# Optimization experiments

Hardware: AMD Instinct MI355X
Metric: run time of the kernel (lower is better)

Reference implementation:

```python
import jax, jax.numpy as jnp
import numpy as np
from math import factorial

# ---- static config: mirrors FullTensorProductSparse("64x0e + 64x1o", "32x0e + 32x1o", leading_shape=(2048,)) ----
IRREPS1 = [(64, 0, 1), (64, 1, -1)]   # (mul, l, parity); already regrouped
IRREPS2 = [(32, 0, 1), (32, 1, -1)]
N_LEAD = 2048


def _su2_cg_coeff(j1, m1, j2, m2, j3, m3):
    # Racah formula, identical to e3nn._su2_clebsch_gordan_coeff
    if m3 != m1 + m2:
        return 0.0
    f = factorial
    vmin = max(-j1 + j2 + m3, -j1 + m1, 0)
    vmax = min(j2 + j3 + m1, j3 - j1 + j2, j3 + m3)
    C = ((2.0 * j3 + 1.0) * f(j3 + j1 - j2) * f(j3 - j1 + j2) * f(j1 + j2 - j3)
         * f(j3 + m3) * f(j3 - m3)
         / (f(j1 + j2 + j3 + 1) * f(j1 - m1) * f(j1 + m1) * f(j2 - m2) * f(j2 + m2))) ** 0.5
    S = 0.0
    for v in range(vmin, vmax + 1):
        S += (-1.0) ** (v + j2 + m2) * f(j2 + j3 + m1 - v) * f(j1 - m1 + v) / (
            f(v) * f(j3 - j1 + j2 - v) * f(j3 + m3 - v) * f(v + j1 - j2 - m3))
    return C * S


def _su2_cg(j1, j2, j3):
    mat = np.zeros((2 * j1 + 1, 2 * j2 + 1, 2 * j3 + 1), dtype=np.float64)
    if abs(j1 - j2) <= j3 <= j1 + j2:
        for m1 in range(-j1, j1 + 1):
            for m2 in range(-j2, j2 + 1):
                if abs(m1 + m2) <= j3:
                    mat[j1 + m1, j2 + m2, j3 + m1 + m2] = _su2_cg_coeff(j1, m1, j2, m2, j3, m1 + m2)
    return mat / (2 * j3 + 1) ** 0.5


def _change_basis_real_to_complex(l):
    q = np.zeros((2 * l + 1, 2 * l + 1), dtype=np.complex128)
    for m in range(-l, 0):
        q[l + m, l + abs(m)] = 2 ** -0.5
        q[l + m, l - abs(m)] = -1j * 2 ** -0.5
    q[l, l] = 1.0
    for m in range(1, l + 1):
        q[l + m, l + abs(m)] = (-1) ** m * 2 ** -0.5
        q[l + m, l - abs(m)] = 1j * (-1) ** m * 2 ** -0.5
    return (-1j) ** l * q  # phase makes the real-basis CG coefficients real


def wigner_3j(l1, l2, l3):
    # real-basis Wigner 3j, identical to e3nn.o3.wigner_3j
    Q1 = _change_basis_real_to_complex(l1)
    Q2 = _change_basis_real_to_complex(l2)
    Q3 = _change_basis_real_to_complex(l3)
    C = _su2_cg(l1, l2, l3).astype(np.complex128)
    C = np.einsum('ij,kl,mn,ikn->jlm', Q1, Q2, np.conj(Q3.T), C)
    assert np.abs(C.imag).max() < 1e-8
    C = C.real
    return C / np.linalg.norm(C)


def _paths():
    # mirrors the (l1,l2,l3) path construction in __init__ (no filter_ir_out)
    paths = []
    off1 = 0
    for mul1, l1, p1 in IRREPS1:
        d1 = 2 * l1 + 1
        off2 = 0
        for mul2, l2, p2 in IRREPS2:
            d2 = 2 * l2 + 1
            for l3 in range(abs(l1 - l2), l1 + l2 + 1):
                p3 = p1 * p2
                cg = wigner_3j(l1, l2, l3) * np.sqrt(2 * l3 + 1)  # 'component' normalization
                paths.append((off1, mul1, d1, off2, mul2, d2, l3, p3, cg))
            off2 += mul2 * d2
        off1 += mul1 * d1
    return paths


def setup_inputs() -> dict:
    key = jax.random.key(0)
    k1, k2 = jax.random.split(key)
    d_in1 = sum(m * (2 * l + 1) for m, l, _ in IRREPS1)
    d_in2 = sum(m * (2 * l + 1) for m, l, _ in IRREPS2)
    return {
        'input1': jax.random.normal(k1, (N_LEAD, d_in1), dtype=jnp.float32),
        'input2': jax.random.normal(k2, (N_LEAD, d_in2), dtype=jnp.float32),
    }


def reference(input1, input2):
    n = input1.shape[0]
    chunks, keys = [], []
    for off1, mul1, d1, off2, mul2, d2, l3, p3, cg in _paths():
        d3 = 2 * l3 + 1
        # faithful to the torch module: raw row-major reshape of the (n, mul*dim)
        # irrep slice into (dim, mul, n) (no transpose), exactly as in forward().
        x1 = input1[:, off1:off1 + mul1 * d1].reshape(d1, mul1, n)
        x2 = input2[:, off2:off2 + mul2 * d2].reshape(d2, mul2, n)
        C = jnp.asarray(cg, dtype=input1.dtype)
        # dense CG contraction == the sparse (m1,m2,m3) loop: CG is zero off-pattern
        chunk = jnp.einsum('ijk,iun,jvn->kuvn', C, x1, x2)  # [d3, mul1, mul2, n]
        chunk = jnp.moveaxis(chunk, 0, -1).reshape(n, mul1 * mul2 * d3)
        chunks.append(chunk)
        keys.append((l3, -p3 * (-1) ** l3))  # Irrep canonical sort key: 0e,0o,1o,1e,2e,2o
    inv = sorted(range(len(keys)), key=lambda i: keys[i])  # stable argsort == Irreps.sort().inv
    return jnp.concatenate([chunks[i] for i in inv], axis=-1)
```

## Files before the change

kernel.cpp:

```cpp
#include <hip/hip_runtime.h>
#include <complex>
#include <cmath>


static double fct(int n) { double r = 1.0; for (int i = 2; i <= n; ++i) r *= i; return r; }

static double su2_cg_coeff(int j1, int m1, int j2, int m2, int j3, int m3) {
    if (m3 != m1 + m2) return 0.0;
    int vmin = std::max(std::max(-j1 + j2 + m3, -j1 + m1), 0);
    int vmax = std::min(std::min(j2 + j3 + m1, j3 - j1 + j2), j3 + m3);
    double C = std::sqrt((2.0 * j3 + 1.0) * fct(j3 + j1 - j2) * fct(j3 - j1 + j2) * fct(j1 + j2 - j3)
                         * fct(j3 + m3) * fct(j3 - m3)
                         / (fct(j1 + j2 + j3 + 1) * fct(j1 - m1) * fct(j1 + m1) * fct(j2 - m2) * fct(j2 + m2)));
    double S = 0.0;
    for (int v = vmin; v <= vmax; ++v) {
        double sgn = ((v + j2 + m2) & 1) ? -1.0 : 1.0;
        S += sgn * fct(j2 + j3 + m1 - v) * fct(j1 - m1 + v)
             / (fct(v) * fct(j3 - j1 + j2 - v) * fct(j3 + m3 - v) * fct(v + j1 - j2 - m3));
    }
    return C * S;
}

static void cob(int l, std::complex<double> q[5][5]) {
    for (int a = 0; a < 5; ++a) for (int b = 0; b < 5; ++b) q[a][b] = 0.0;
    const double is2 = 1.0 / std::sqrt(2.0);
    for (int m = -l; m < 0; ++m) {
        q[l + m][l - m] = is2;
        q[l + m][l + m] = std::complex<double>(0.0, -is2);
    }
    q[l][l] = 1.0;
    for (int m = 1; m <= l; ++m) {
        double sgn = (m & 1) ? -1.0 : 1.0;
        q[l + m][l + m] = sgn * is2;
        q[l + m][l - m] = std::complex<double>(0.0, sgn * is2);
    }
    std::complex<double> ph;
    switch (l & 3) {
        case 0: ph = 1.0; break;
        case 1: ph = std::complex<double>(0.0, -1.0); break;
        case 2: ph = -1.0; break;
        default: ph = std::complex<double>(0.0, 1.0); break;
    }
    for (int a = 0; a < 5; ++a) for (int b = 0; b < 5; ++b) q[a][b] *= ph;
}

static void wigner3j(int l1, int l2, int l3, double* out) {
    int d1 = 2 * l1 + 1, d2 = 2 * l2 + 1, d3 = 2 * l3 + 1;
    double csu2[5][5][5] = {};
    for (int m1 = -l1; m1 <= l1; ++m1)
        for (int m2 = -l2; m2 <= l2; ++m2)
            if (std::abs(m1 + m2) <= l3)
                csu2[l1 + m1][l2 + m2][l3 + m1 + m2] =
                    su2_cg_coeff(l1, m1, l2, m2, l3, m1 + m2) / std::sqrt(2.0 * l3 + 1.0);
    std::complex<double> Q1[5][5], Q2[5][5], Q3[5][5];
    cob(l1, Q1); cob(l2, Q2); cob(l3, Q3);
    double nrm = 0.0;
    for (int j = 0; j < d1; ++j)
        for (int l = 0; l < d2; ++l)
            for (int m = 0; m < d3; ++m) {
                std::complex<double> s = 0.0;
                for (int i = 0; i < d1; ++i)
                    for (int k = 0; k < d2; ++k)
                        for (int n = 0; n < d3; ++n)
                            s += Q1[i][j] * Q2[k][l] * std::conj(Q3[n][m]) * csu2[i][k][n];
                out[(j * d2 + l) * d3 + m] = s.real();
                nrm += s.real() * s.real();
            }
    nrm = std::sqrt(nrm);
    for (int t = 0; t < d1 * d2 * d3; ++t) out[t] /= nrm;
}

struct CGTab {
    float cA;
    float B[9];
    float Cjk[9];
    float Dik[9];
    float E[27];
    float F[45];
};


__global__ __launch_bounds__(256) void ftp_kernel(const float* __restrict__ in1,
                                                  const float* __restrict__ in2,
                                                  float* __restrict__ out,
                                                  CGTab cg) {
    __shared__ float lds[4096];

    const int t   = threadIdx.x;
    const int nn0 = blockIdx.x * 256;
    const int nn  = nn0 + t;
    const int r   = blockIdx.y;
    const int u   = r >> 5;
    const int v   = r & 31;

    const float a0 = in1[(u * 32 + (nn >> 6)) * 256 + (nn & 63)];
    const float b0 = in2[(v * 64 + (nn >> 5)) * 128 + (nn & 31)];

    float a1[3], b1[3];
#pragma unroll
    for (int i = 0; i < 3; ++i) {
        int f = i * 131072 + u * 2048 + nn;
        int row = f / 192, col = f - row * 192;
        a1[i] = in1[row * 256 + 64 + col];
    }
#pragma unroll
    for (int j = 0; j < 3; ++j) {
        int g = j * 65536 + v * 2048 + nn;
        int row = g / 96, col = g - row * 96;
        b1[j] = in2[row * 128 + 32 + col];
    }

    lds[t] = cg.cA * a0 * b0;

    {
        float s = 0.f;
#pragma unroll
        for (int i = 0; i < 3; ++i)
#pragma unroll
            for (int j = 0; j < 3; ++j)
                s = fmaf(cg.B[i * 3 + j], a1[i] * b1[j], s);
        lds[256 + t] = s;
    }

#pragma unroll
    for (int k = 0; k < 3; ++k) {
        float s = 0.f;
#pragma unroll
        for (int j = 0; j < 3; ++j) s = fmaf(cg.Cjk[j * 3 + k], b1[j], s);
        lds[512 + t * 3 + k] = a0 * s;
    }

#pragma unroll
    for (int k = 0; k < 3; ++k) {
        float s = 0.f;
#pragma unroll
        for (int i = 0; i < 3; ++i) s = fmaf(cg.Dik[i * 3 + k], a1[i], s);
        lds[1280 + t * 3 + k] = b0 * s;
    }

#pragma unroll
    for (int k = 0; k < 3; ++k) {
        float s = 0.f;
#pragma unroll
        for (int i = 0; i < 3; ++i)
#pragma unroll
            for (int j = 0; j < 3; ++j)
                s = fmaf(cg.E[(i * 3 + j) * 3 + k], a1[i] * b1[j], s);
        lds[2048 + t * 3 + k] = s;
    }

#pragma unroll
    for (int k = 0; k < 5; ++k) {
        float s = 0.f;
#pragma unroll
        for (int i = 0; i < 3; ++i)
#pragma unroll
            for (int j = 0; j < 3; ++j)
                s = fmaf(cg.F[(i * 3 + j) * 5 + k], a1[i] * b1[j], s);
        lds[2816 + t * 5 + k] = s;
    }

    __syncthreads();

    const float4* lv = (const float4*)lds;
    float4* orow4 = (float4*)(out + (size_t)r * 32768);
    const int q4 = nn0 >> 2;

#pragma unroll
    for (int s = 0; s < 4; ++s) {
        const int q = t + s * 256;
        int g;
        if      (q < 64)  g = 0    + q4     + q;
        else if (q < 128) g = 512  + q4     + (q - 64);
        else if (q < 320) g = 1024 + 3 * q4 + (q - 128);
        else if (q < 512) g = 2560 + 3 * q4 + (q - 320);
        else if (q < 704) g = 4096 + 3 * q4 + (q - 512);
        else              g = 5632 + 5 * q4 + (q - 704);
        orow4[g] = lv[q];
    }
}


extern "C" void kernel_launch(void* const* d_in, const int* in_sizes, int n_in,
                              void* d_out, int out_size, void* d_ws, size_t ws_size,
                              hipStream_t stream) {
    const float* in1 = (const float*)d_in[0];
    const float* in2 = (const float*)d_in[1];
    float* out = (float*)d_out;

    CGTab cg;
    double w[45];
    const double s3 = std::sqrt(3.0), s5 = std::sqrt(5.0);

    wigner3j(0, 0, 0, w);
    cg.cA = (float)(w[0] * 1.0);

    wigner3j(1, 1, 0, w);
    for (int i = 0; i < 3; ++i)
        for (int j = 0; j < 3; ++j) cg.B[i * 3 + j] = (float)(w[(i * 3 + j)] * 1.0);

    wigner3j(0, 1, 1, w);
    for (int j = 0; j < 3; ++j)
        for (int k = 0; k < 3; ++k) cg.Cjk[j * 3 + k] = (float)(w[j * 3 + k] * s3);

    wigner3j(1, 0, 1, w);
    for (int i = 0; i < 3; ++i)
        for (int k = 0; k < 3; ++k) cg.Dik[i * 3 + k] = (float)(w[i * 3 + k] * s3);

    wigner3j(1, 1, 1, w);
    for (int t = 0; t < 27; ++t) cg.E[t] = (float)(w[t] * s3);

    wigner3j(1, 1, 2, w);
    for (int t = 0; t < 45; ++t) cg.F[t] = (float)(w[t] * s5);

    dim3 grid(2048 / 256, 2048, 1);
    dim3 block(256, 1, 1);
    ftp_kernel<<<grid, block, 0, stream>>>(in1, in2, out, cg);
}
```

Baseline: 262.1 us.

## Drop LDS staging; each thread computes four points and writes float4 directly

The kernel no longer stages results in shared memory with a barrier. Each block now owns a full output row (2048 points), and each thread handles four consecutive points per half. Inputs are read with float4 loads and each path's outputs are written straight to global memory as contiguous float4 stores. This removes the LDS round-trip and __syncthreads, and cuts the grid to 2048 blocks. In exchange it raises per-thread register use and the scattered float4 stores may coalesce less well than the old staged layout.

```diff
diff --git a/kernel.cpp b/kernel.cpp
--- a/kernel.cpp
+++ b/kernel.cpp
@@ -84,99 +84,107 @@
                                                   const float* __restrict__ in2,
                                                   float* __restrict__ out,
                                                   CGTab cg) {
-    __shared__ float lds[4096];
-
-    const int t   = threadIdx.x;
-    const int nn0 = blockIdx.x * 256;
-    const int nn  = nn0 + t;
-    const int r   = blockIdx.y;
-    const int u   = r >> 5;
-    const int v   = r & 31;
-
-    const float a0 = in1[(u * 32 + (nn >> 6)) * 256 + (nn & 63)];
-    const float b0 = in2[(v * 64 + (nn >> 5)) * 128 + (nn & 31)];
-
-    float a1[3], b1[3];
-#pragma unroll
-    for (int i = 0; i < 3; ++i) {
-        int f = i * 131072 + u * 2048 + nn;
-        int row = f / 192, col = f - row * 192;
-        a1[i] = in1[row * 256 + 64 + col];
-    }
-#pragma unroll
-    for (int j = 0; j < 3; ++j) {
-        int g = j * 65536 + v * 2048 + nn;
-        int row = g / 96, col = g - row * 96;
-        b1[j] = in2[row * 128 + 32 + col];
-    }
-
-    lds[t] = cg.cA * a0 * b0;
-
-    {
-        float s = 0.f;
-#pragma unroll
-        for (int i = 0; i < 3; ++i)
-#pragma unroll
-            for (int j = 0; j < 3; ++j)
-                s = fmaf(cg.B[i * 3 + j], a1[i] * b1[j], s);
-        lds[256 + t] = s;
-    }
-
-#pragma unroll
-    for (int k = 0; k < 3; ++k) {
-        float s = 0.f;
-#pragma unroll
-        for (int j = 0; j < 3; ++j) s = fmaf(cg.Cjk[j * 3 + k], b1[j], s);
-        lds[512 + t * 3 + k] = a0 * s;
-    }
-
-#pragma unroll
-    for (int k = 0; k < 3; ++k) {
-        float s = 0.f;
-#pragma unroll
-        for (int i = 0; i < 3; ++i) s = fmaf(cg.Dik[i * 3 + k], a1[i], s);
-        lds[1280 + t * 3 + k] = b0 * s;
-    }
-
-#pragma unroll
-    for (int k = 0; k < 3; ++k) {
-        float s = 0.f;
-#pragma unroll
-        for (int i = 0; i < 3; ++i)
-#pragma unroll
-            for (int j = 0; j < 3; ++j)
-                s = fmaf(cg.E[(i * 3 + j) * 3 + k], a1[i] * b1[j], s);
-        lds[2048 + t * 3 + k] = s;
-    }
-
-#pragma unroll
-    for (int k = 0; k < 5; ++k) {
-        float s = 0.f;
-#pragma unroll
-        for (int i = 0; i < 3; ++i)
-#pragma unroll
-            for (int j = 0; j < 3; ++j)
-                s = fmaf(cg.F[(i * 3 + j) * 5 + k], a1[i] * b1[j], s);
-        lds[2816 + t * 5 + k] = s;
-    }
-
-    __syncthreads();
-
-    const float4* lv = (const float4*)lds;
-    float4* orow4 = (float4*)(out + (size_t)r * 32768);
-    const int q4 = nn0 >> 2;
-
-#pragma unroll
-    for (int s = 0; s < 4; ++s) {
-        const int q = t + s * 256;
-        int g;
-        if      (q < 64)  g = 0    + q4     + q;
-        else if (q < 128) g = 512  + q4     + (q - 64);
-        else if (q < 320) g = 1024 + 3 * q4 + (q - 128);
-        else if (q < 512) g = 2560 + 3 * q4 + (q - 320);
-        else if (q < 704) g = 4096 + 3 * q4 + (q - 512);
-        else              g = 5632 + 5 * q4 + (q - 704);
-        orow4[g] = lv[q];
+    const int t = threadIdx.x;
+    const int r = blockIdx.x;
+    const int u = r >> 5;
+    const int v = r & 31;
+    float* __restrict__ orow = out + (size_t)r * 32768;
+
+#pragma unroll
+    for (int h = 0; h < 2; ++h) {
+        const int nn = h * 1024 + t * 4;
+
+        alignas(16) float a0q[4], b0q[4], a1q[3][4], b1q[3][4];
+        *(float4*)a0q = *(const float4*)&in1[(u * 32 + (nn >> 6)) * 256 + (nn & 63)];
+        *(float4*)b0q = *(const float4*)&in2[(v * 64 + (nn >> 5)) * 128 + (nn & 31)];
+#pragma unroll
+        for (int i = 0; i < 3; ++i) {
+            const int f   = i * 131072 + u * 2048 + nn;
+            const int row = f / 192, col = f - row * 192;
+            *(float4*)a1q[i] = *(const float4*)&in1[row * 256 + 64 + col];
+        }
+#pragma unroll
+        for (int j = 0; j < 3; ++j) {
+            const int g   = j * 65536 + v * 2048 + nn;
+            const int row = g / 96, col = g - row * 96;
+            *(float4*)b1q[j] = *(const float4*)&in2[row * 128 + 32 + col];
+        }
+
+        alignas(16) float o[20];
+
+#pragma unroll
+        for (int d = 0; d < 4; ++d) o[d] = cg.cA * a0q[d] * b0q[d];
+        *(float4*)&orow[nn] = *(const float4*)o;
+
+#pragma unroll
+        for (int d = 0; d < 4; ++d) {
+            float s = 0.f;
+#pragma unroll
+            for (int i = 0; i < 3; ++i)
+#pragma unroll
+                for (int j = 0; j < 3; ++j)
+                    s = fmaf(cg.B[i * 3 + j], a1q[i][d] * b1q[j][d], s);
+            o[d] = s;
+        }
+        *(float4*)&orow[2048 + nn] = *(const float4*)o;
+
+#pragma unroll
+        for (int d = 0; d < 4; ++d)
+#pragma unroll
+            for (int k = 0; k < 3; ++k) {
+                float s = 0.f;
+#pragma unroll
+                for (int j = 0; j < 3; ++j) s = fmaf(cg.Cjk[j * 3 + k], b1q[j][d], s);
+                o[d * 3 + k] = a0q[d] * s;
+            }
+#pragma unroll
+        for (int s4 = 0; s4 < 3; ++s4)
+            *(float4*)&orow[4096 + 3 * nn + 4 * s4] = *(const float4*)&o[4 * s4];
+
+#pragma unroll
+        for (int d = 0; d < 4; ++d)
+#pragma unroll
+            for (int k = 0; k < 3; ++k) {
+                float s = 0.f;
+#pragma unroll
+                for (int i = 0; i < 3; ++i) s = fmaf(cg.Dik[i * 3 + k], a1q[i][d], s);
+                o[d * 3 + k] = b0q[d] * s;
+            }
+#pragma unroll
+        for (int s4 = 0; s4 < 3; ++s4)
+            *(float4*)&orow[10240 + 3 * nn + 4 * s4] = *(const float4*)&o[4 * s4];
+
+#pragma unroll
+        for (int d = 0; d < 4; ++d)
+#pragma unroll
+            for (int k = 0; k < 3; ++k) {
+                float s = 0.f;
+#pragma unroll
+                for (int i = 0; i < 3; ++i)
+#pragma unroll
+                    for (int j = 0; j < 3; ++j)
+                        s = fmaf(cg.E[(i * 3 + j) * 3 + k], a1q[i][d] * b1q[j][d], s);
+                o[d * 3 + k] = s;
+            }
+#pragma unroll
+        for (int s4 = 0; s4 < 3; ++s4)
+            *(float4*)&orow[16384 + 3 * nn + 4 * s4] = *(const float4*)&o[4 * s4];
+
+#pragma unroll
+        for (int d = 0; d < 4; ++d)
+#pragma unroll
+            for (int k = 0; k < 5; ++k) {
+                float s = 0.f;
+#pragma unroll
+                for (int i = 0; i < 3; ++i)
+#pragma unroll
+                    for (int j = 0; j < 3; ++j)
+                        s = fmaf(cg.F[(i * 3 + j) * 5 + k], a1q[i][d] * b1q[j][d], s);
+                o[d * 5 + k] = s;
+            }
+#pragma unroll
+        for (int s4 = 0; s4 < 5; ++s4)
+            *(float4*)&orow[22528 + 5 * nn + 4 * s4] = *(const float4*)&o[4 * s4];
     }
 }
 
@@ -213,7 +221,7 @@
     wigner3j(1, 1, 2, w);
     for (int t = 0; t < 45; ++t) cg.F[t] = (float)(w[t] * s5);
 
-    dim3 grid(2048 / 256, 2048, 1);
+    dim3 grid(2048, 1, 1);
     dim3 block(256, 1, 1);
     ftp_kernel<<<grid, block, 0, stream>>>(in1, in2, out, cg);
 }
```

New measurement: 299.8 us. 1.14x slower.
